# Kernel optimization log

Hardware: AMD Instinct MI355X
Metric: run time of the kernel (lower is better)

The kernel has to match this reference:

```python
import jax, jax.numpy as jnp
import numpy as np
import math

H = 8                 # num_heads
MAX_REL = 32          # max_relative_distance
VOCAB_REL = 2 * MAX_REL + 1


def setup_inputs() -> dict:
    key = jax.random.key(0)
    ks = jax.random.split(key, 8)
    B, S, D = 4, 2048, 256
    hd = D // H
    sd = 1.0 / math.sqrt(D)
    inp = {
        "query": jax.random.normal(ks[0], (B, S, D), jnp.float32),
        "mask": jnp.ones((B, 1, 1, S), jnp.float32),
        "Wq": jax.random.normal(ks[1], (D, D), jnp.float32) * sd,
        "bq": jnp.zeros((D,), jnp.float32),
        "Wk": jax.random.normal(ks[2], (D, D), jnp.float32) * sd,
        "bk": jnp.zeros((D,), jnp.float32),
        "Wv": jax.random.normal(ks[3], (D, D), jnp.float32) * sd,
        "bv": jnp.zeros((D,), jnp.float32),
        "Wo": jax.random.normal(ks[4], (D, D), jnp.float32) * sd,
        "bo": jnp.zeros((D,), jnp.float32),
        "rel_table": jax.random.normal(ks[5], (VOCAB_REL, hd), jnp.float32) * 0.1,
    }
    return inp


def _split_heads(x, B, S, hd):
    # [B,S,D] -> [B,H,S,hd]
    return x.reshape(B, S, H, hd).transpose(0, 2, 1, 3)


def _relative_row_sums(S, rel_table):
    # Original: emb = table[relpos]  (S,S,hd); scores += einsum('bhid,jkd->bhijk', Q, emb).sum(-1)
    # == einsum('bhid,jd->bhij', Q, R) with R[j,d] = sum_k emb[j,k,d].
    # Compute R without materializing the (S,S,hd) tensor: count how often each
    # relative-position bucket appears in each row, then counts @ table.
    pos = jnp.arange(S)
    relpos = jnp.clip(pos[:, None] - pos[None, :], -MAX_REL, MAX_REL) + MAX_REL  # [S,S] ints
    rows = jnp.broadcast_to(pos[:, None], (S, S))
    counts = jnp.zeros((S, VOCAB_REL), rel_table.dtype).at[
        rows.reshape(-1), relpos.reshape(-1)
    ].add(1.0)
    return counts @ rel_table  # [S, hd]


def reference(query, mask, Wq, bq, Wk, bk, Wv, bv, Wo, bo, rel_table):
    B, S, D = query.shape
    hd = D // H
    scale = 1.0 / math.sqrt(hd)

    Q = _split_heads(query @ Wq + bq, B, S, hd)
    K = _split_heads(query @ Wk + bk, B, S, hd)   # key defaults to query
    V = _split_heads(query @ Wv + bv, B, S, hd)   # value defaults to key

    scores = jnp.einsum("bhid,bhjd->bhij", Q, K) * scale
    R = _relative_row_sums(S, rel_table)          # [S, hd]
    scores = scores + jnp.einsum("bhid,jd->bhij", Q, R)

    scores = scores + (1.0 - mask) * -1e9         # mask broadcast [B,1,1,S]
    attn = jax.nn.softmax(scores, axis=-1)        # dropout is identity (training=False)

    out = jnp.einsum("bhij,bhjd->bhid", attn, V)
    out = out.transpose(0, 2, 1, 3).reshape(B, S, D)
    return out @ Wo + bo
```

## Files before the change

### kernel.cpp

```cpp
#include <hip/hip_runtime.h>
#include <hip/hip_bf16.h>
#include <math.h>

#define NH 8
#define HD 32
#define SEQ 2048
#define DM 256
#define SCALE 0.17677669529663687f
#define INV_SCALE 5.656854249492381f
#define LOG2E 1.4426950408889634f
#define QSC (SCALE * LOG2E)
#define MNEG (-1e9f * LOG2E)

typedef float f32x4 __attribute__((ext_vector_type(4)));
typedef __bf16 bf16x8 __attribute__((ext_vector_type(8)));

#define GLOAD(g, l) __builtin_amdgcn_global_load_lds( \
    (const __attribute__((address_space(1))) void*)(g), \
    (__attribute__((address_space(3))) void*)(l), 16, 0, 0)

__global__ void k_prep(const float* __restrict__ query, const float* __restrict__ mask,
                       const float* __restrict__ Wq, const float* __restrict__ Wk,
                       const float* __restrict__ Wv, const float* __restrict__ Wo,
                       const float* __restrict__ bq, const float* __restrict__ tbl,
                       __bf16* __restrict__ Xb, __bf16* __restrict__ Wt,
                       __bf16* __restrict__ WoT, float* __restrict__ MT,
                       __bf16* __restrict__ SUFn, __bf16* __restrict__ PREn,
                       float* __restrict__ WV2T, float* __restrict__ cb,
                       int* __restrict__ MFLAG) {
  const int blk = blockIdx.x, tid = threadIdx.x;
  __shared__ float ts[64][65];
  __shared__ int okl;
  if (blk < 1024) {
    size_t i = (size_t)blk * 2048 + (size_t)tid * 8;
    float4 a = *(const float4*)(query + i);
    float4 b4 = *(const float4*)(query + i + 4);
    union { __bf16 h[8]; bf16x8 v; } o;
    o.h[0] = (__bf16)a.x;  o.h[1] = (__bf16)a.y;
    o.h[2] = (__bf16)a.z;  o.h[3] = (__bf16)a.w;
    o.h[4] = (__bf16)b4.x; o.h[5] = (__bf16)b4.y;
    o.h[6] = (__bf16)b4.z; o.h[7] = (__bf16)b4.w;
    *(bf16x8*)(Xb + i) = o.v;
  } else if (blk < 1088) {
    const int idx = blk - 1024;
    const float* W;
    __bf16* dst;
    int tile;
    if (idx < 48) {
      int which = idx >> 4;
      W = which == 0 ? Wq : (which == 1 ? Wk : Wv);
      dst = Wt + which * 65536;
      tile = idx & 15;
    } else {
      W = Wo; dst = WoT; tile = idx - 48;
    }
    const int tr = (tile >> 2) * 64, tc = (tile & 3) * 64;
#pragma unroll
    for (int p = 0; p < 4; ++p) {
      int row = p * 16 + (tid >> 4);
      int col = (tid & 15) * 4;
      float4 v = *(const float4*)(W + (size_t)(tr + row) * 256 + tc + col);
      ts[row][col] = v.x; ts[row][col + 1] = v.y;
      ts[row][col + 2] = v.z; ts[row][col + 3] = v.w;
    }
    __syncthreads();
#pragma unroll
    for (int p = 0; p < 2; ++p) {
      int n = p * 32 + (tid >> 3);
      int kb = (tid & 7) * 8;
      union { __bf16 h[8]; bf16x8 v; } o;
#pragma unroll
      for (int e = 0; e < 8; ++e) o.h[e] = (__bf16)ts[kb + e][n];
      *(bf16x8*)(dst + (size_t)(tc + n) * 256 + tr + kb) = o.v;
    }
  } else if (blk == 1088) {
    if (tid == 0) okl = 1;
    __syncthreads();
    bool ok = true;
    for (int i = tid; i < 4 * SEQ; i += 256) {
      float mv = mask[i];
      MT[i] = (1.0f - mv) * MNEG;
      ok &= (mv == 1.0f);
    }
    if (!ok) atomicAnd(&okl, 0);
    __syncthreads();
    if (tid == 0) MFLAG[0] = okl;
  } else if (blk == 1089) {
    for (int idx = tid; idx < 1024; idx += 256) {
      int j = idx >> 5, d = idx & 31;
      float s = 0.f;
      for (int u = j + 33; u <= 63; ++u) s += tbl[u * 32 + d];
      SUFn[idx] = (__bf16)(-s * INV_SCALE);
    }
    for (int idx = tid; idx < 1024; idx += 256) {
      int jj = idx >> 5, d = idx & 31;
      float s = 0.f;
      for (int u = 1; u <= jj; ++u) s += tbl[u * 32 + d];
      PREn[idx] = (__bf16)(-s * INV_SCALE);
    }
  } else if (blk < 1106) {
    int tg = (blk - 1090) * 256 + tid;
    int hv = tg >> 8, k = tg & 255;
    const float* T = tbl + ((hv & 1) ? 0 : 64 * 32);
    const float* w = Wq + (size_t)k * 256 + (hv >> 1) * 32;
    float acc = 0.f;
#pragma unroll
    for (int d = 0; d < 32; ++d) acc = fmaf(w[d], T[d], acc);
    WV2T[hv * 256 + k] = acc * LOG2E;
  } else {
    if (tid < 16) {
      const float* T = tbl + ((tid & 1) ? 0 : 64 * 32);
      float a = 0.f;
#pragma unroll
      for (int d = 0; d < 32; ++d) a = fmaf(bq[(tid >> 1) * 32 + d], T[d], a);
      cb[tid] = a * LOG2E;
    }
  }
}

__launch_bounds__(256)
__global__ void k_rel(const float* __restrict__ X, const float* __restrict__ WV2T,
                      const float* __restrict__ cb, float* __restrict__ REL) {
  __shared__ float Xs[32][260];
  __shared__ float Ws[16][260];
  const int tid = threadIdx.x;
  const size_t base = (size_t)blockIdx.x * 32 * 256;
#pragma unroll
  for (int p = 0; p < 8; ++p) {
    int idx = p * 1024 + tid * 4;
    float4 v = *(const float4*)(X + base + idx);
    *(float4*)&Xs[idx >> 8][idx & 255] = v;
  }
#pragma unroll
  for (int p = 0; p < 4; ++p) {
    int idx = p * 1024 + tid * 4;
    float4 v = *(const float4*)(WV2T + idx);
    *(float4*)&Ws[idx >> 8][idx & 255] = v;
  }
  __syncthreads();
  const int hv = tid & 15, rl = tid >> 4;
  float a0 = cb[hv], a1 = a0;
  const float* xs0 = &Xs[rl][0];
  const float* xs1 = &Xs[rl + 16][0];
  const float* wsp = &Ws[hv][0];
#pragma unroll 8
  for (int k = 0; k < 256; ++k) {
    float w = wsp[k];
    a0 = fmaf(xs0[k], w, a0);
    a1 = fmaf(xs1[k], w, a1);
  }
  const int row0 = blockIdx.x * 32 + rl;
  const int h = hv >> 1, v = hv & 1;
  const int b0i = row0 >> 11, s0 = row0 & 2047;
  REL[((size_t)(b0i * NH + h) * SEQ + s0) * 2 + v] = a0;
  const int r1 = row0 + 16;
  const int b1i = r1 >> 11, s1 = r1 & 2047;
  REL[((size_t)(b1i * NH + h) * SEQ + s1) * 2 + v] = a1;
}

template <int MODE>
__launch_bounds__(256)
__global__ void k_gemm(const __bf16* __restrict__ A, const __bf16* __restrict__ Bt,
                       const float* __restrict__ b0, const float* __restrict__ b1,
                       const float* __restrict__ b2,
                       __bf16* __restrict__ Qb, __bf16* __restrict__ Kb,
                       __bf16* __restrict__ VTout, float* __restrict__ Y) {
  constexpr int BN = (MODE == 0) ? 128 : 64;
  constexpr int NFJ = BN / 32;
  __shared__ __align__(16) __bf16 As[128 * 64];
  __shared__ __align__(16) __bf16 Bs[BN * 64];
  const int tid = threadIdx.x, lane = tid & 63, wid = tid >> 6;
  const int l16 = lane & 15, lhi = lane >> 4;
  const int wr = wid >> 1, wc = wid & 1;
  const int m0 = blockIdx.x * 128, n0 = blockIdx.y * BN;

  f32x4 acc[4][NFJ];
#pragma unroll
  for (int i = 0; i < 4; ++i)
#pragma unroll
    for (int j = 0; j < NFJ; ++j) acc[i][j] = (f32x4){0.f, 0.f, 0.f, 0.f};

  for (int k0 = 0; k0 < 256; k0 += 64) {
    __syncthreads();
#pragma unroll
    for (int cc = 0; cc < 4; ++cc) {
      int cl = tid + cc * 256;
      int row = cl >> 3, kc = cl & 7;
      int k = k0 + ((kc ^ (row & 7)) * 8);
      const __bf16* src;
      if constexpr (MODE == 0) {
        src = A + (size_t)(m0 + row) * 256 + k;
      } else {
        int r = m0 + row, bb = r >> 11, s = r & 2047, h = k >> 5, dh = k & 31;
        src = A + ((size_t)(bb * NH + h) * SEQ + s) * HD + dh;
      }
      GLOAD(src, (__bf16*)As + (size_t)cl * 8);
    }
#pragma unroll
    for (int cc = 0; cc < NFJ; ++cc) {
      int cl = tid + cc * 256;
      int row = cl >> 3, kc = cl & 7;
      int k = k0 + ((kc ^ (row & 7)) * 8);
      GLOAD(Bt + (size_t)(n0 + row) * 256 + k, (__bf16*)Bs + (size_t)cl * 8);
    }
    __syncthreads();
#pragma unroll
    for (int kk = 0; kk < 64; kk += 32) {
      bf16x8 af[4], bfr[NFJ];
#pragma unroll
      for (int fi = 0; fi < 4; ++fi) {
        int row = wr * 64 + fi * 16 + l16;
        af[fi] = *(const bf16x8*)(As + row * 64 + ((((kk >> 3) + lhi) ^ (row & 7)) * 8));
      }
#pragma unroll
      for (int fj = 0; fj < NFJ; ++fj) {
        int row = wc * (BN / 2) + fj * 16 + l16;
        bfr[fj] = *(const bf16x8*)(Bs + row * 64 + ((((kk >> 3) + lhi) ^ (row & 7)) * 8));
      }
#pragma unroll
      for (int fi = 0; fi < 4; ++fi)
#pragma unroll
        for (int fj = 0; fj < NFJ; ++fj)
          acc[fi][fj] = __builtin_amdgcn_mfma_f32_16x16x32_bf16(af[fi], bfr[fj], acc[fi][fj], 0, 0, 0);
    }
  }
#pragma unroll
  for (int fi = 0; fi < 4; ++fi) {
#pragma unroll
    for (int fj = 0; fj < NFJ; ++fj) {
      int mrow = m0 + wr * 64 + fi * 16 + lhi * 4;
      int ncol = n0 + wc * (BN / 2) + fj * 16 + l16;
      if constexpr (MODE == 0) {
        int which = ncol >> 8, nw = ncol & 255, h = nw >> 5, dh = nw & 31;
        int bb = mrow >> 11, s0 = mrow & 2047;
        if (which == 2) {
          union { __bf16 h4[4]; uint2 u; } o;
#pragma unroll
          for (int r = 0; r < 4; ++r) o.h4[r] = (__bf16)(acc[fi][fj][r] + b2[nw]);
          *(uint2*)(VTout + ((size_t)(bb * NH + h) * HD + dh) * SEQ + s0) = o.u;
        } else {
          const float* bias = which == 0 ? b0 : b1;
#pragma unroll
          for (int r = 0; r < 4; ++r) {
            float v = acc[fi][fj][r] + bias[nw];
            size_t oi = ((size_t)(bb * NH + h) * SEQ + (s0 + r)) * HD + dh;
            if (which == 0) Qb[oi] = (__bf16)(v * QSC);
            else Kb[oi] = (__bf16)v;
          }
        }
      } else {
#pragma unroll
        for (int r = 0; r < 4; ++r)
          Y[(size_t)(mrow + r) * 256 + ncol] = acc[fi][fj][r] + b0[ncol];
      }
    }
  }
}

__launch_bounds__(512, 4)
__global__ void k_flash(const __bf16* __restrict__ Qb, const __bf16* __restrict__ Kb,
                        const __bf16* __restrict__ VT, const float* __restrict__ REL,
                        const __bf16* __restrict__ SUFn, const __bf16* __restrict__ PREn,
                        const float* __restrict__ MT, const int* __restrict__ MFLAG,
                        __bf16* __restrict__ Ob) {
  const int bh = blockIdx.y, qt = blockIdx.x, b = bh >> 3;
  const int tid = threadIdx.x, wid = tid >> 6, lane = tid & 63;
  const int l16 = lane & 15, lhi = lane >> 4;

  __shared__ __align__(16) __bf16 kbuf[2][128 * 32];
  __shared__ __align__(16) __bf16 vbuf[2][32 * 128];
  __shared__ __align__(16) __bf16 plds[8][16 * 128];

  const int qrow = qt * 128 + wid * 16 + l16;
  const size_t rg = (size_t)bh * SEQ + qrow;
  const bf16x8 qfrag = *(const bf16x8*)(Qb + rg * HD + lhi * 8);
  const float2 uw = *(const float2*)(REL + rg * 2);
  const float uu = uw.x, ww = uw.y, duw = uu - ww;
  const float duw16 = 16.f * duw;
  const f32x4 duwr = {0.f, duw, 2.f * duw, 3.f * duw};
  const int flag = MFLAG[0];

  const int kj = tid >> 2, kc = tid & 3;
  const __bf16* ksrc = Kb + (size_t)bh * SEQ * HD + (size_t)kj * HD + ((kc ^ ((kj >> 1) & 3)) * 8);
  const int vd = tid >> 4, vc = tid & 15;
  const __bf16* vsrc = VT + ((size_t)bh * HD + vd) * SEQ + ((vc ^ (vd & 7)) * 8);

  f32x4 of0 = {0.f, 0.f, 0.f, 0.f}, of1 = {0.f, 0.f, 0.f, 0.f}, of2 = {0.f, 0.f, 0.f, 0.f};
  const f32x4 zero4 = {0.f, 0.f, 0.f, 0.f}; (void)zero4;
  bf16x8 ones;
#pragma unroll
  for (int e = 0; e < 8; ++e) ones[e] = (__bf16)1.0f;
  float m = -3.0e38f;
  __bf16* pl = &plds[wid][0];
  const float* mtp = MT + b * SEQ + lhi * 4;

  GLOAD(ksrc, &kbuf[0][(size_t)tid * 8]);
  GLOAD(vsrc, &vbuf[0][(size_t)tid * 8]);
  __syncthreads();

  for (int t = 0, cur = 0; t < 16; ++t, cur ^= 1) {
    const int jb = t * 128;
    if (t < 15) {
      GLOAD(ksrc + (size_t)(jb + 128) * HD, &kbuf[cur ^ 1][(size_t)tid * 8]);
      GLOAD(vsrc + (jb + 128), &vbuf[cur ^ 1][(size_t)tid * 8]);
    }
    const __bf16* kb = kbuf[cur];
    const __bf16* vb = vbuf[cur];

    f32x4 lin = duwr + (float)(jb + lhi * 4) * duw;
    f32x4 sf[8];
    __builtin_amdgcn_s_setprio(1);
#pragma unroll
    for (int jt = 0; jt < 8; ++jt) {
      const int row = jt * 16 + l16;
      bf16x8 kf = *(const bf16x8*)(kb + row * 32 + ((lhi ^ ((row >> 1) & 3)) * 8));
      sf[jt] = __builtin_amdgcn_mfma_f32_16x16x32_bf16(kf, qfrag, lin, 0, 0, 0);
      lin += duw16;
    }
    __builtin_amdgcn_s_setprio(0);

    if (t == 0) {
      const bf16x8 s0 = *(const bf16x8*)(SUFn + l16 * HD + lhi * 8);
      const bf16x8 s1 = *(const bf16x8*)(SUFn + (16 + l16) * HD + lhi * 8);
      sf[0] = __builtin_amdgcn_mfma_f32_16x16x32_bf16(s0, qfrag, sf[0], 0, 0, 0);
      sf[1] = __builtin_amdgcn_mfma_f32_16x16x32_bf16(s1, qfrag, sf[1], 0, 0, 0);
#pragma unroll
      for (int jt = 0; jt < 2; ++jt)
#pragma unroll
        for (int r = 0; r < 4; ++r)
          sf[jt][r] += fmaxf(31.f - (float)(jt * 16 + lhi * 4 + r), 0.f) * uu;
    }
    if (t == 15) {
      const bf16x8 p0 = *(const bf16x8*)(PREn + l16 * HD + lhi * 8);
      const bf16x8 p1 = *(const bf16x8*)(PREn + (16 + l16) * HD + lhi * 8);
      sf[6] = __builtin_amdgcn_mfma_f32_16x16x32_bf16(p0, qfrag, sf[6], 0, 0, 0);
      sf[7] = __builtin_amdgcn_mfma_f32_16x16x32_bf16(p1, qfrag, sf[7], 0, 0, 0);
#pragma unroll
      for (int jt = 6; jt < 8; ++jt)
#pragma unroll
        for (int r = 0; r < 4; ++r)
          sf[jt][r] += fmaxf((float)(1920 + jt * 16 + lhi * 4 + r) - 2016.f, 0.f) * ww;
    }
    if (!flag) {
#pragma unroll
      for (int jt = 0; jt < 8; ++jt)
        sf[jt] += *(const f32x4*)(mtp + jb + jt * 16);
    }

    float tmax = -3.0e38f;
#pragma unroll
    for (int jt = 0; jt < 8; ++jt)
      tmax = fmaxf(tmax, fmaxf(fmaxf(sf[jt].x, sf[jt].y), fmaxf(sf[jt].z, sf[jt].w)));
    tmax = fmaxf(tmax, __shfl_xor(tmax, 16));
    tmax = fmaxf(tmax, __shfl_xor(tmax, 32));
    const float mn = fmaxf(m, tmax);
    const float c = __builtin_amdgcn_exp2f(m - mn);
    m = mn;
    of0 *= c; of1 *= c; of2 *= c;

#pragma unroll
    for (int jt = 0; jt < 8; ++jt) {
      union { __bf16 h4[4]; uint2 u; } pk;
#pragma unroll
      for (int r = 0; r < 4; ++r)
        pk.h4[r] = (__bf16)__builtin_amdgcn_exp2f(sf[jt][r] - m);
      const int blk16 = ((jt * 2 + (lhi >> 1)) ^ (l16 & 7));
      *(uint2*)(pl + l16 * 128 + blk16 * 8 + (lhi & 1) * 4) = pk.u;
    }

    __builtin_amdgcn_s_setprio(1);
#pragma unroll
    for (int kt = 0; kt < 4; ++kt) {
      const int pblk = (kt * 4 + lhi) ^ (l16 & 7);
      bf16x8 pf = *(const bf16x8*)(pl + l16 * 128 + pblk * 8);
      bf16x8 v0 = *(const bf16x8*)(vb + l16 * 128 + (((kt * 4 + lhi) ^ (l16 & 7)) * 8));
      bf16x8 v1 = *(const bf16x8*)(vb + (16 + l16) * 128 + (((kt * 4 + lhi) ^ (l16 & 7)) * 8));
      of0 = __builtin_amdgcn_mfma_f32_16x16x32_bf16(v0, pf, of0, 0, 0, 0);
      of1 = __builtin_amdgcn_mfma_f32_16x16x32_bf16(v1, pf, of1, 0, 0, 0);
      of2 = __builtin_amdgcn_mfma_f32_16x16x32_bf16(ones, pf, of2, 0, 0, 0);
    }
    __builtin_amdgcn_s_setprio(0);
    __syncthreads();
  }

  const float inv = 1.0f / of2[0];
  union { __bf16 h4[4]; uint2 u; } o0, o1;
#pragma unroll
  for (int r = 0; r < 4; ++r) {
    o0.h4[r] = (__bf16)(of0[r] * inv);
    o1.h4[r] = (__bf16)(of1[r] * inv);
  }
  *(uint2*)(Ob + rg * HD + lhi * 4) = o0.u;
  *(uint2*)(Ob + rg * HD + 16 + lhi * 4) = o1.u;
}

extern "C" void kernel_launch(void* const* d_in, const int* in_sizes, int n_in,
                              void* d_out, int out_size, void* d_ws, size_t ws_size,
                              hipStream_t stream) {
  (void)in_sizes; (void)n_in; (void)out_size; (void)ws_size;
  const float* query = (const float*)d_in[0];
  const float* mask  = (const float*)d_in[1];
  const float* Wq = (const float*)d_in[2];
  const float* bq = (const float*)d_in[3];
  const float* Wk = (const float*)d_in[4];
  const float* bk = (const float*)d_in[5];
  const float* Wv = (const float*)d_in[6];
  const float* bv = (const float*)d_in[7];
  const float* Wo = (const float*)d_in[8];
  const float* bo = (const float*)d_in[9];
  const float* tbl = (const float*)d_in[10];
  float* out = (float*)d_out;
  char* ws = (char*)d_ws;

  const size_t MB = 1024ull * 1024;
  __bf16* Xb    = (__bf16*)(ws);
  __bf16* Wt    = (__bf16*)(ws + 4 * MB);
  __bf16* WoT   = (__bf16*)(ws + 4 * MB + 393216);
  __bf16* SUFn  = (__bf16*)(ws + 4 * MB + 524288);
  __bf16* PREn  = (__bf16*)(ws + 4 * MB + 526336);
  float*  WV2T  = (float*) (ws + 4 * MB + 528384);
  float*  cbv   = (float*) (ws + 4 * MB + 544768);
  float*  MT    = (float*) (ws + 4 * MB + 544832);
  int*    MFLAG = (int*)   (ws + 4 * MB + 577600);
  float*  REL   = (float*) (ws + 5 * MB);
  __bf16* Qb    = (__bf16*)(ws + 6 * MB);
  __bf16* Kb    = (__bf16*)(ws + 10 * MB);
  __bf16* VT    = (__bf16*)(ws + 14 * MB);
  __bf16* Ob    = (__bf16*)(ws + 18 * MB);

  k_prep<<<1107, 256, 0, stream>>>(query, mask, Wq, Wk, Wv, Wo, bq, tbl,
                                   Xb, Wt, WoT, MT, SUFn, PREn, WV2T, cbv, MFLAG);
  k_rel<<<256, 256, 0, stream>>>(query, WV2T, cbv, REL);
  k_gemm<0><<<dim3(64, 6), 256, 0, stream>>>(Xb, Wt, bq, bk, bv, Qb, Kb, VT, nullptr);
  k_flash<<<dim3(16, 32), 512, 0, stream>>>(Qb, Kb, VT, REL, SUFn, PREn, MT, MFLAG, Ob);
  k_gemm<1><<<dim3(64, 4), 256, 0, stream>>>(Ob, WoT, bo, nullptr, nullptr,
                                             nullptr, nullptr, nullptr, out);
}
```

Baseline: 89.65 us.

## Fuse bf16 cast into k_rel, retile GEMMs, and double flash K/V tile

```diff
diff --git a/kernel.cpp b/kernel.cpp
--- a/kernel.cpp
+++ b/kernel.cpp
@@ -19,30 +19,20 @@
     (const __attribute__((address_space(1))) void*)(g), \
     (__attribute__((address_space(3))) void*)(l), 16, 0, 0)
 
-__global__ void k_prep(const float* __restrict__ query, const float* __restrict__ mask,
+__global__ void k_prep(const float* __restrict__ mask,
                        const float* __restrict__ Wq, const float* __restrict__ Wk,
                        const float* __restrict__ Wv, const float* __restrict__ Wo,
                        const float* __restrict__ bq, const float* __restrict__ tbl,
-                       __bf16* __restrict__ Xb, __bf16* __restrict__ Wt,
-                       __bf16* __restrict__ WoT, float* __restrict__ MT,
+                       __bf16* __restrict__ Wt, __bf16* __restrict__ WoT,
+                       float* __restrict__ MT,
                        __bf16* __restrict__ SUFn, __bf16* __restrict__ PREn,
                        float* __restrict__ WV2T, float* __restrict__ cb,
                        int* __restrict__ MFLAG) {
   const int blk = blockIdx.x, tid = threadIdx.x;
   __shared__ float ts[64][65];
   __shared__ int okl;
-  if (blk < 1024) {
-    size_t i = (size_t)blk * 2048 + (size_t)tid * 8;
-    float4 a = *(const float4*)(query + i);
-    float4 b4 = *(const float4*)(query + i + 4);
-    union { __bf16 h[8]; bf16x8 v; } o;
-    o.h[0] = (__bf16)a.x;  o.h[1] = (__bf16)a.y;
-    o.h[2] = (__bf16)a.z;  o.h[3] = (__bf16)a.w;
-    o.h[4] = (__bf16)b4.x; o.h[5] = (__bf16)b4.y;
-    o.h[6] = (__bf16)b4.z; o.h[7] = (__bf16)b4.w;
-    *(bf16x8*)(Xb + i) = o.v;
-  } else if (blk < 1088) {
-    const int idx = blk - 1024;
+  if (blk < 64) {
+    const int idx = blk;
     const float* W;
     __bf16* dst;
     int tile;
@@ -73,7 +63,7 @@
       for (int e = 0; e < 8; ++e) o.h[e] = (__bf16)ts[kb + e][n];
       *(bf16x8*)(dst + (size_t)(tc + n) * 256 + tr + kb) = o.v;
     }
-  } else if (blk == 1088) {
+  } else if (blk == 64) {
     if (tid == 0) okl = 1;
     __syncthreads();
     bool ok = true;
@@ -85,7 +75,7 @@
     if (!ok) atomicAnd(&okl, 0);
     __syncthreads();
     if (tid == 0) MFLAG[0] = okl;
-  } else if (blk == 1089) {
+  } else if (blk == 65) {
     for (int idx = tid; idx < 1024; idx += 256) {
       int j = idx >> 5, d = idx & 31;
       float s = 0.f;
@@ -98,8 +88,8 @@
       for (int u = 1; u <= jj; ++u) s += tbl[u * 32 + d];
       PREn[idx] = (__bf16)(-s * INV_SCALE);
     }
-  } else if (blk < 1106) {
-    int tg = (blk - 1090) * 256 + tid;
+  } else if (blk < 82) {
+    int tg = (blk - 66) * 256 + tid;
     int hv = tg >> 8, k = tg & 255;
     const float* T = tbl + ((hv & 1) ? 0 : 64 * 32);
     const float* w = Wq + (size_t)k * 256 + (hv >> 1) * 32;
@@ -120,7 +110,8 @@
 
 __launch_bounds__(256)
 __global__ void k_rel(const float* __restrict__ X, const float* __restrict__ WV2T,
-                      const float* __restrict__ cb, float* __restrict__ REL) {
+                      const float* __restrict__ cb, float* __restrict__ REL,
+                      __bf16* __restrict__ Xb) {
   __shared__ float Xs[32][260];
   __shared__ float Ws[16][260];
   const int tid = threadIdx.x;
@@ -138,6 +129,19 @@
     *(float4*)&Ws[idx >> 8][idx & 255] = v;
   }
   __syncthreads();
+#pragma unroll
+  for (int p = 0; p < 4; ++p) {
+    int idx = p * 2048 + tid * 8;
+    int row = idx >> 8, col = idx & 255;
+    float4 a = *(const float4*)&Xs[row][col];
+    float4 b4 = *(const float4*)&Xs[row][col + 4];
+    union { __bf16 h[8]; bf16x8 v; } o;
+    o.h[0] = (__bf16)a.x;  o.h[1] = (__bf16)a.y;
+    o.h[2] = (__bf16)a.z;  o.h[3] = (__bf16)a.w;
+    o.h[4] = (__bf16)b4.x; o.h[5] = (__bf16)b4.y;
+    o.h[6] = (__bf16)b4.z; o.h[7] = (__bf16)b4.w;
+    *(bf16x8*)(Xb + base + idx) = o.v;
+  }
   const int hv = tid & 15, rl = tid >> 4;
   float a0 = cb[hv], a1 = a0;
   const float* xs0 = &Xs[rl][0];
@@ -165,25 +169,25 @@
                        const float* __restrict__ b2,
                        __bf16* __restrict__ Qb, __bf16* __restrict__ Kb,
                        __bf16* __restrict__ VTout, float* __restrict__ Y) {
-  constexpr int BN = (MODE == 0) ? 128 : 64;
-  constexpr int NFJ = BN / 32;
-  __shared__ __align__(16) __bf16 As[128 * 64];
-  __shared__ __align__(16) __bf16 Bs[BN * 64];
+  constexpr int BM = (MODE == 0) ? 128 : 64;
+  constexpr int FI = BM / 32;
+  __shared__ __align__(16) __bf16 As[BM * 64];
+  __shared__ __align__(16) __bf16 Bs[64 * 64];
   const int tid = threadIdx.x, lane = tid & 63, wid = tid >> 6;
   const int l16 = lane & 15, lhi = lane >> 4;
   const int wr = wid >> 1, wc = wid & 1;
-  const int m0 = blockIdx.x * 128, n0 = blockIdx.y * BN;
-
-  f32x4 acc[4][NFJ];
-#pragma unroll
-  for (int i = 0; i < 4; ++i)
-#pragma unroll
-    for (int j = 0; j < NFJ; ++j) acc[i][j] = (f32x4){0.f, 0.f, 0.f, 0.f};
+  const int m0 = blockIdx.x * BM, n0 = blockIdx.y * 64;
+
+  f32x4 acc[FI][2];
+#pragma unroll
+  for (int i = 0; i < FI; ++i)
+#pragma unroll
+    for (int j = 0; j < 2; ++j) acc[i][j] = (f32x4){0.f, 0.f, 0.f, 0.f};
 
   for (int k0 = 0; k0 < 256; k0 += 64) {
     __syncthreads();
 #pragma unroll
-    for (int cc = 0; cc < 4; ++cc) {
+    for (int cc = 0; cc < BM / 32; ++cc) {
       int cl = tid + cc * 256;
       int row = cl >> 3, kc = cl & 7;
       int k = k0 + ((kc ^ (row & 7)) * 8);
@@ -197,7 +201,7 @@
       GLOAD(src, (__bf16*)As + (size_t)cl * 8);
     }
 #pragma unroll
-    for (int cc = 0; cc < NFJ; ++cc) {
+    for (int cc = 0; cc < 2; ++cc) {
       int cl = tid + cc * 256;
       int row = cl >> 3, kc = cl & 7;
       int k = k0 + ((kc ^ (row & 7)) * 8);
@@ -206,30 +210,30 @@
     __syncthreads();
 #pragma unroll
     for (int kk = 0; kk < 64; kk += 32) {
-      bf16x8 af[4], bfr[NFJ];
-#pragma unroll
-      for (int fi = 0; fi < 4; ++fi) {
-        int row = wr * 64 + fi * 16 + l16;
+      bf16x8 af[FI], bfr[2];
+#pragma unroll
+      for (int fi = 0; fi < FI; ++fi) {
+        int row = wr * (BM / 2) + fi * 16 + l16;
         af[fi] = *(const bf16x8*)(As + row * 64 + ((((kk >> 3) + lhi) ^ (row & 7)) * 8));
       }
 #pragma unroll
-      for (int fj = 0; fj < NFJ; ++fj) {
-        int row = wc * (BN / 2) + fj * 16 + l16;
+      for (int fj = 0; fj < 2; ++fj) {
+        int row = wc * 32 + fj * 16 + l16;
         bfr[fj] = *(const bf16x8*)(Bs + row * 64 + ((((kk >> 3) + lhi) ^ (row & 7)) * 8));
       }
 #pragma unroll
-      for (int fi = 0; fi < 4; ++fi)
-#pragma unroll
-        for (int fj = 0; fj < NFJ; ++fj)
+      for (int fi = 0; fi < FI; ++fi)
+#pragma unroll
+        for (int fj = 0; fj < 2; ++fj)
           acc[fi][fj] = __builtin_amdgcn_mfma_f32_16x16x32_bf16(af[fi], bfr[fj], acc[fi][fj], 0, 0, 0);
     }
   }
 #pragma unroll
-  for (int fi = 0; fi < 4; ++fi) {
-#pragma unroll
-    for (int fj = 0; fj < NFJ; ++fj) {
-      int mrow = m0 + wr * 64 + fi * 16 + lhi * 4;
-      int ncol = n0 + wc * (BN / 2) + fj * 16 + l16;
+  for (int fi = 0; fi < FI; ++fi) {
+#pragma unroll
+    for (int fj = 0; fj < 2; ++fj) {
+      int mrow = m0 + wr * (BM / 2) + fi * 16 + lhi * 4;
+      int ncol = n0 + wc * 32 + fj * 16 + l16;
       if constexpr (MODE == 0) {
         int which = ncol >> 8, nw = ncol & 255, h = nw >> 5, dh = nw & 31;
         int bb = mrow >> 11, s0 = mrow & 2047;
@@ -263,13 +267,16 @@
                         const __bf16* __restrict__ SUFn, const __bf16* __restrict__ PREn,
                         const float* __restrict__ MT, const int* __restrict__ MFLAG,
                         __bf16* __restrict__ Ob) {
-  const int bh = blockIdx.y, qt = blockIdx.x, b = bh >> 3;
+  const int bid = blockIdx.x;
+  const int bh = (bid & 7) * 4 + ((bid >> 3) & 3);
+  const int qt = bid >> 5;
+  const int b = bh >> 3;
   const int tid = threadIdx.x, wid = tid >> 6, lane = tid & 63;
   const int l16 = lane & 15, lhi = lane >> 4;
 
-  __shared__ __align__(16) __bf16 kbuf[2][128 * 32];
-  __shared__ __align__(16) __bf16 vbuf[2][32 * 128];
-  __shared__ __align__(16) __bf16 plds[8][16 * 128];
+  __shared__ __align__(16) __bf16 kbuf[2][256 * 32];
+  __shared__ __align__(16) __bf16 vbuf[2][32 * 256];
+  __shared__ __align__(16) __bf16 plds[8][16 * 64];
 
   const int qrow = qt * 128 + wid * 16 + l16;
   const size_t rg = (size_t)bh * SEQ + qrow;
@@ -280,13 +287,15 @@
   const f32x4 duwr = {0.f, duw, 2.f * duw, 3.f * duw};
   const int flag = MFLAG[0];
 
-  const int kj = tid >> 2, kc = tid & 3;
-  const __bf16* ksrc = Kb + (size_t)bh * SEQ * HD + (size_t)kj * HD + ((kc ^ ((kj >> 1) & 3)) * 8);
-  const int vd = tid >> 4, vc = tid & 15;
-  const __bf16* vsrc = VT + ((size_t)bh * HD + vd) * SEQ + ((vc ^ (vd & 7)) * 8);
+  const int u0 = tid, u1 = tid + 512;
+  const int kj0 = u0 >> 2, kc0 = u0 & 3, kj1 = u1 >> 2, kc1 = u1 & 3;
+  const __bf16* ksrc0 = Kb + ((size_t)bh * SEQ + kj0) * HD + ((kc0 ^ ((kj0 >> 1) & 3)) * 8);
+  const __bf16* ksrc1 = Kb + ((size_t)bh * SEQ + kj1) * HD + ((kc1 ^ ((kj1 >> 1) & 3)) * 8);
+  const int vd0 = u0 >> 5, vc0 = u0 & 31, vd1 = u1 >> 5, vc1 = u1 & 31;
+  const __bf16* vsrc0 = VT + ((size_t)bh * HD + vd0) * SEQ + ((vc0 ^ (vd0 & 7)) * 8);
+  const __bf16* vsrc1 = VT + ((size_t)bh * HD + vd1) * SEQ + ((vc1 ^ (vd1 & 7)) * 8);
 
   f32x4 of0 = {0.f, 0.f, 0.f, 0.f}, of1 = {0.f, 0.f, 0.f, 0.f}, of2 = {0.f, 0.f, 0.f, 0.f};
-  const f32x4 zero4 = {0.f, 0.f, 0.f, 0.f}; (void)zero4;
   bf16x8 ones;
 #pragma unroll
   for (int e = 0; e < 8; ++e) ones[e] = (__bf16)1.0f;
@@ -294,92 +303,104 @@
   __bf16* pl = &plds[wid][0];
   const float* mtp = MT + b * SEQ + lhi * 4;
 
-  GLOAD(ksrc, &kbuf[0][(size_t)tid * 8]);
-  GLOAD(vsrc, &vbuf[0][(size_t)tid * 8]);
+  GLOAD(ksrc0, &kbuf[0][(size_t)u0 * 8]);
+  GLOAD(ksrc1, &kbuf[0][(size_t)u1 * 8]);
+  GLOAD(vsrc0, &vbuf[0][(size_t)u0 * 8]);
+  GLOAD(vsrc1, &vbuf[0][(size_t)u1 * 8]);
   __syncthreads();
 
-  for (int t = 0, cur = 0; t < 16; ++t, cur ^= 1) {
-    const int jb = t * 128;
-    if (t < 15) {
-      GLOAD(ksrc + (size_t)(jb + 128) * HD, &kbuf[cur ^ 1][(size_t)tid * 8]);
-      GLOAD(vsrc + (jb + 128), &vbuf[cur ^ 1][(size_t)tid * 8]);
+  for (int mt = 0, cur = 0; mt < 8; ++mt, cur ^= 1) {
+    if (mt < 7) {
+      const int nb = cur ^ 1;
+      GLOAD(ksrc0 + (size_t)(mt + 1) * 8192, &kbuf[nb][(size_t)u0 * 8]);
+      GLOAD(ksrc1 + (size_t)(mt + 1) * 8192, &kbuf[nb][(size_t)u1 * 8]);
+      GLOAD(vsrc0 + (mt + 1) * 256, &vbuf[nb][(size_t)u0 * 8]);
+      GLOAD(vsrc1 + (mt + 1) * 256, &vbuf[nb][(size_t)u1 * 8]);
     }
     const __bf16* kb = kbuf[cur];
     const __bf16* vb = vbuf[cur];
 
-    f32x4 lin = duwr + (float)(jb + lhi * 4) * duw;
-    f32x4 sf[8];
-    __builtin_amdgcn_s_setprio(1);
-#pragma unroll
-    for (int jt = 0; jt < 8; ++jt) {
-      const int row = jt * 16 + l16;
-      bf16x8 kf = *(const bf16x8*)(kb + row * 32 + ((lhi ^ ((row >> 1) & 3)) * 8));
-      sf[jt] = __builtin_amdgcn_mfma_f32_16x16x32_bf16(kf, qfrag, lin, 0, 0, 0);
-      lin += duw16;
-    }
-    __builtin_amdgcn_s_setprio(0);
-
-    if (t == 0) {
-      const bf16x8 s0 = *(const bf16x8*)(SUFn + l16 * HD + lhi * 8);
-      const bf16x8 s1 = *(const bf16x8*)(SUFn + (16 + l16) * HD + lhi * 8);
-      sf[0] = __builtin_amdgcn_mfma_f32_16x16x32_bf16(s0, qfrag, sf[0], 0, 0, 0);
-      sf[1] = __builtin_amdgcn_mfma_f32_16x16x32_bf16(s1, qfrag, sf[1], 0, 0, 0);
-#pragma unroll
-      for (int jt = 0; jt < 2; ++jt)
-#pragma unroll
-        for (int r = 0; r < 4; ++r)
-          sf[jt][r] += fmaxf(31.f - (float)(jt * 16 + lhi * 4 + r), 0.f) * uu;
-    }
-    if (t == 15) {
-      const bf16x8 p0 = *(const bf16x8*)(PREn + l16 * HD + lhi * 8);
-      const bf16x8 p1 = *(const bf16x8*)(PREn + (16 + l16) * HD + lhi * 8);
-      sf[6] = __builtin_amdgcn_mfma_f32_16x16x32_bf16(p0, qfrag, sf[6], 0, 0, 0);
-      sf[7] = __builtin_amdgcn_mfma_f32_16x16x32_bf16(p1, qfrag, sf[7], 0, 0, 0);
-#pragma unroll
-      for (int jt = 6; jt < 8; ++jt)
-#pragma unroll
-        for (int r = 0; r < 4; ++r)
-          sf[jt][r] += fmaxf((float)(1920 + jt * 16 + lhi * 4 + r) - 2016.f, 0.f) * ww;
-    }
-    if (!flag) {
+#pragma unroll
+    for (int sub = 0; sub < 2; ++sub) {
+      const int jb = mt * 256 + sub * 128;
+
+      f32x4 lin = duwr + (float)(jb + lhi * 4) * duw;
+      f32x4 sf[8];
+      __builtin_amdgcn_s_setprio(1);
+#pragma unroll
+      for (int jt = 0; jt < 8; ++jt) {
+        const int row = sub * 128 + jt * 16 + l16;
+        bf16x8 kf = *(const bf16x8*)(kb + row * 32 + ((lhi ^ ((row >> 1) & 3)) * 8));
+        sf[jt] = __builtin_amdgcn_mfma_f32_16x16x32_bf16(kf, qfrag, lin, 0, 0, 0);
+        lin += duw16;
+      }
+      __builtin_amdgcn_s_setprio(0);
+
+      if (jb == 0) {
+        const bf16x8 s0 = *(const bf16x8*)(SUFn + l16 * HD + lhi * 8);
+        const bf16x8 s1 = *(const bf16x8*)(SUFn + (16 + l16) * HD + lhi * 8);
+        sf[0] = __builtin_amdgcn_mfma_f32_16x16x32_bf16(s0, qfrag, sf[0], 0, 0, 0);
+        sf[1] = __builtin_amdgcn_mfma_f32_16x16x32_bf16(s1, qfrag, sf[1], 0, 0, 0);
+#pragma unroll
+        for (int jt = 0; jt < 2; ++jt)
+#pragma unroll
+          for (int r = 0; r < 4; ++r)
+            sf[jt][r] += fmaxf(31.f - (float)(jt * 16 + lhi * 4 + r), 0.f) * uu;
+      }
+      if (jb == SEQ - 128) {
+        const bf16x8 p0 = *(const bf16x8*)(PREn + l16 * HD + lhi * 8);
+        const bf16x8 p1 = *(const bf16x8*)(PREn + (16 + l16) * HD + lhi * 8);
+        sf[6] = __builtin_amdgcn_mfma_f32_16x16x32_bf16(p0, qfrag, sf[6], 0, 0, 0);
+        sf[7] = __builtin_amdgcn_mfma_f32_16x16x32_bf16(p1, qfrag, sf[7], 0, 0, 0);
+#pragma unroll
+        for (int jt = 6; jt < 8; ++jt)
+#pragma unroll
+          for (int r = 0; r < 4; ++r)
+            sf[jt][r] += fmaxf((float)(jb + jt * 16 + lhi * 4 + r) - 2016.f, 0.f) * ww;
+      }
+      if (!flag) {
+#pragma unroll
+        for (int jt = 0; jt < 8; ++jt)
+          sf[jt] += *(const f32x4*)(mtp + jb + jt * 16);
+      }
+
+      float tmax = -3.0e38f;
 #pragma unroll
       for (int jt = 0; jt < 8; ++jt)
-        sf[jt] += *(const f32x4*)(mtp + jb + jt * 16);
-    }
-
-    float tmax = -3.0e38f;
-#pragma unroll
-    for (int jt = 0; jt < 8; ++jt)
-      tmax = fmaxf(tmax, fmaxf(fmaxf(sf[jt].x, sf[jt].y), fmaxf(sf[jt].z, sf[jt].w)));
-    tmax = fmaxf(tmax, __shfl_xor(tmax, 16));
-    tmax = fmaxf(tmax, __shfl_xor(tmax, 32));
-    const float mn = fmaxf(m, tmax);
-    const float c = __builtin_amdgcn_exp2f(m - mn);
-    m = mn;
-    of0 *= c; of1 *= c; of2 *= c;
-
-#pragma unroll
-    for (int jt = 0; jt < 8; ++jt) {
-      union { __bf16 h4[4]; uint2 u; } pk;
-#pragma unroll
-      for (int r = 0; r < 4; ++r)
-        pk.h4[r] = (__bf16)__builtin_amdgcn_exp2f(sf[jt][r] - m);
-      const int blk16 = ((jt * 2 + (lhi >> 1)) ^ (l16 & 7));
-      *(uint2*)(pl + l16 * 128 + blk16 * 8 + (lhi & 1) * 4) = pk.u;
-    }
-
-    __builtin_amdgcn_s_setprio(1);
-#pragma unroll
-    for (int kt = 0; kt < 4; ++kt) {
-      const int pblk = (kt * 4 + lhi) ^ (l16 & 7);
-      bf16x8 pf = *(const bf16x8*)(pl + l16 * 128 + pblk * 8);
-      bf16x8 v0 = *(const bf16x8*)(vb + l16 * 128 + (((kt * 4 + lhi) ^ (l16 & 7)) * 8));
-      bf16x8 v1 = *(const bf16x8*)(vb + (16 + l16) * 128 + (((kt * 4 + lhi) ^ (l16 & 7)) * 8));
-      of0 = __builtin_amdgcn_mfma_f32_16x16x32_bf16(v0, pf, of0, 0, 0, 0);
-      of1 = __builtin_amdgcn_mfma_f32_16x16x32_bf16(v1, pf, of1, 0, 0, 0);
-      of2 = __builtin_amdgcn_mfma_f32_16x16x32_bf16(ones, pf, of2, 0, 0, 0);
-    }
-    __builtin_amdgcn_s_setprio(0);
+        tmax = fmaxf(tmax, fmaxf(fmaxf(sf[jt].x, sf[jt].y), fmaxf(sf[jt].z, sf[jt].w)));
+      tmax = fmaxf(tmax, __shfl_xor(tmax, 16));
+      tmax = fmaxf(tmax, __shfl_xor(tmax, 32));
+      const float mn = fmaxf(m, tmax);
+      const float c = __builtin_amdgcn_exp2f(m - mn);
+      m = mn;
+      of0 *= c; of1 *= c; of2 *= c;
+
+#pragma unroll
+      for (int ph = 0; ph < 2; ++ph) {
+#pragma unroll
+        for (int jt = ph * 4; jt < ph * 4 + 4; ++jt) {
+          union { __bf16 h4[4]; uint2 u; } pk;
+#pragma unroll
+          for (int r = 0; r < 4; ++r)
+            pk.h4[r] = (__bf16)__builtin_amdgcn_exp2f(sf[jt][r] - m);
+          const int blk16 = (((jt & 3) * 2 + (lhi >> 1)) ^ (l16 & 7));
+          *(uint2*)(pl + l16 * 64 + blk16 * 8 + (lhi & 1) * 4) = pk.u;
+        }
+        __builtin_amdgcn_s_setprio(1);
+#pragma unroll
+        for (int kt = ph * 2; kt < ph * 2 + 2; ++kt) {
+          const int pblk = (((kt & 1) * 4 + lhi) ^ (l16 & 7));
+          bf16x8 pf = *(const bf16x8*)(pl + l16 * 64 + pblk * 8);
+          const int G = sub * 16 + kt * 4 + lhi;
+          bf16x8 v0 = *(const bf16x8*)(vb + l16 * 256 + ((G ^ (l16 & 7)) * 8));
+          bf16x8 v1 = *(const bf16x8*)(vb + (16 + l16) * 256 + ((G ^ (l16 & 7)) * 8));
+          of0 = __builtin_amdgcn_mfma_f32_16x16x32_bf16(v0, pf, of0, 0, 0, 0);
+          of1 = __builtin_amdgcn_mfma_f32_16x16x32_bf16(v1, pf, of1, 0, 0, 0);
+          of2 = __builtin_amdgcn_mfma_f32_16x16x32_bf16(ones, pf, of2, 0, 0, 0);
+        }
+        __builtin_amdgcn_s_setprio(0);
+      }
+    }
     __syncthreads();
   }
 
@@ -428,11 +449,11 @@
   __bf16* VT    = (__bf16*)(ws + 14 * MB);
   __bf16* Ob    = (__bf16*)(ws + 18 * MB);
 
-  k_prep<<<1107, 256, 0, stream>>>(query, mask, Wq, Wk, Wv, Wo, bq, tbl,
-                                   Xb, Wt, WoT, MT, SUFn, PREn, WV2T, cbv, MFLAG);
-  k_rel<<<256, 256, 0, stream>>>(query, WV2T, cbv, REL);
-  k_gemm<0><<<dim3(64, 6), 256, 0, stream>>>(Xb, Wt, bq, bk, bv, Qb, Kb, VT, nullptr);
-  k_flash<<<dim3(16, 32), 512, 0, stream>>>(Qb, Kb, VT, REL, SUFn, PREn, MT, MFLAG, Ob);
-  k_gemm<1><<<dim3(64, 4), 256, 0, stream>>>(Ob, WoT, bo, nullptr, nullptr,
-                                             nullptr, nullptr, nullptr, out);
+  k_prep<<<83, 256, 0, stream>>>(mask, Wq, Wk, Wv, Wo, bq, tbl,
+                                 Wt, WoT, MT, SUFn, PREn, WV2T, cbv, MFLAG);
+  k_rel<<<256, 256, 0, stream>>>(query, WV2T, cbv, REL, Xb);
+  k_gemm<0><<<dim3(64, 12), 256, 0, stream>>>(Xb, Wt, bq, bk, bv, Qb, Kb, VT, nullptr);
+  k_flash<<<512, 512, 0, stream>>>(Qb, Kb, VT, REL, SUFn, PREn, MT, MFLAG, Ob);
+  k_gemm<1><<<dim3(128, 4), 256, 0, stream>>>(Ob, WoT, bo, nullptr, nullptr,
+                                              nullptr, nullptr, nullptr, out);
 }
```

Result: slower. 92.27 us (+2.9%).
